# Performance work log

Measured on AMD Instinct MI355X. Metric: run time of the kernel, lower is better.

## Reference

```python
import jax, jax.numpy as jnp
import numpy as np

ALPHA = 2.0   # snntorch ATan surrogate default
THRESH = 1.0  # snntorch Leaky default threshold

@jax.custom_vjp
def spike(x):
    return (x > 0).astype(x.dtype)

def _spike_fwd(x):
    return spike(x), x

def _spike_bwd(x, g):
    # ATan surrogate gradient: (alpha/2) / (1 + (pi/2 * alpha * x)^2)
    return (g * (ALPHA / 2) / (1 + (jnp.pi / 2 * ALPHA * x) ** 2),)

spike.defvjp(_spike_fwd, _spike_bwd)

def _lif(inp, mem, beta):
    # snntorch Leaky, reset_mechanism='subtract':
    # reset from previous mem (detached), then integrate, then fire
    reset = jax.lax.stop_gradient(spike(mem - THRESH))
    mem = jnp.clip(beta, 0.0, 1.0) * mem + inp - reset * THRESH
    spk = spike(mem - THRESH)
    return spk, mem

def setup_inputs() -> dict:
    key = jax.random.key(0)
    ks = jax.random.split(key, 8)
    V, H, T, B = 32000, 512, 512, 8
    s = 0.02
    inv = 1.0 / np.sqrt(H)
    return {
        "x": jax.random.randint(ks[0], (T, B), 0, V),
        "emb": jax.random.normal(ks[1], (V, H), jnp.float32) * s,
        "pos_emb": jax.random.normal(ks[2], (T, H), jnp.float32) * s,
        "beta1": jnp.full((H,), 0.9, jnp.float32),
        "beta2": jnp.full((H,), 0.9, jnp.float32),
        "beta3": jnp.full((H,), 0.9, jnp.float32),
        "W2": jax.random.normal(ks[3], (H, H), jnp.float32) * inv,
        "b2": jnp.zeros((H,), jnp.float32),
        "W3": jax.random.normal(ks[4], (H, H), jnp.float32) * inv,
        "b3": jnp.zeros((H,), jnp.float32),
        "Wout": jax.random.normal(ks[5], (V, H), jnp.float32) * inv,
        "bout": jnp.zeros((V,), jnp.float32),
    }

def reference(x, emb, pos_emb, beta1, beta2, beta3, W2, b2, W3, b3, Wout, bout):
    T, B = x.shape
    H = emb.shape[1]
    # precompute token + positional embedding for all steps: [T, B, H]
    hid = emb[x] + pos_emb[:, None, :]
    mem0 = jnp.zeros((B, H), emb.dtype)

    def step(carry, h_t):
        m1, m2, m3 = carry
        spk1, m1 = _lif(h_t, m1, beta1)
        h = jax.nn.relu(spk1 @ W2.T + b2)
        spk2, m2 = _lif(h, m2, beta2)
        h = jax.nn.relu(spk2 @ W3.T + b3)
        spk3, m3 = _lif(h, m3, beta3)
        logits = spk3 @ Wout.T + bout  # [B, V]
        return (m1, m2, m3), logits

    _, out = jax.lax.scan(step, (mem0, mem0, mem0), hid)
    return out  # [T, B, V]
```

## Files before the change

### kernel.cpp

```cpp
#include <hip/hip_runtime.h>

#define TT 512
#define BB 8
#define HH 512
#define VV 32000
#define RR (TT * BB)

typedef float v4f __attribute__((ext_vector_type(4)));

__device__ __forceinline__ float clip01(float x) { return fminf(fmaxf(x, 0.0f), 1.0f); }

__global__ void __launch_bounds__(512) snn_scan_kernel(
        const int* __restrict__ x, const float* __restrict__ emb,
        const float* __restrict__ pos,
        const float* __restrict__ beta1, const float* __restrict__ beta2,
        const float* __restrict__ beta3,
        const float* __restrict__ W2, const float* __restrict__ b2,
        const float* __restrict__ W3, const float* __restrict__ b3,
        int* __restrict__ act1, int* __restrict__ act2, int* __restrict__ act3,
        int* __restrict__ cnt3_g) {
    __shared__ int x_lds[TT];
    __shared__ int c1[TT], c2[TT], c3[TT];
    const int b = blockIdx.x;
    const int h = threadIdx.x;

    x_lds[h] = x[h * BB + b];
    c1[h] = 0; c2[h] = 0; c3[h] = 0;
    __syncthreads();

    {
        float bt = clip01(beta1[h]);
        float m = 0.0f;
        for (int t0 = 0; t0 < TT; t0 += 32) {
            float ev[32], pv[32];
#pragma unroll
            for (int u = 0; u < 32; ++u) {
                int xv = x_lds[t0 + u];
                ev[u] = emb[((size_t)xv << 9) + h];
                pv[u] = pos[((t0 + u) << 9) + h];
            }
#pragma unroll
            for (int u = 0; u < 32; ++u) {
                float inp = ev[u] + pv[u];
                float reset = (m > 1.0f) ? 1.0f : 0.0f;
                m = bt * m + inp - reset;
                if (m > 1.0f) {
                    int t = t0 + u;
                    int p = atomicAdd(&c1[t], 1);
                    act1[((t * BB + b) << 9) + p] = h;
                }
            }
        }
    }
    __syncthreads();

    {
        float bh = b2[h];
        float inp0 = fmaxf(bh, 0.0f);
        float bt = clip01(beta2[h]);
        float m = 0.0f;
        for (int t0 = 0; t0 < TT; t0 += 16) {
            int n[16];
#pragma unroll
            for (int u = 0; u < 16; ++u) n[u] = c1[t0 + u];
#pragma unroll
            for (int u = 0; u < 16; ++u) {
                float inp;
                if (n[u] == 0) {
                    inp = inp0;
                } else {
                    float acc = bh;
                    const int* a = act1 + (((t0 + u) * BB + b) << 9);
                    for (int i = 0; i < n[u]; ++i) acc += W2[(h << 9) + a[i]];
                    inp = fmaxf(acc, 0.0f);
                }
                float reset = (m > 1.0f) ? 1.0f : 0.0f;
                m = bt * m + inp - reset;
                if (m > 1.0f) {
                    int t = t0 + u;
                    int p = atomicAdd(&c2[t], 1);
                    act2[((t * BB + b) << 9) + p] = h;
                }
            }
        }
    }
    __syncthreads();

    {
        float bh = b3[h];
        float inp0 = fmaxf(bh, 0.0f);
        float bt = clip01(beta3[h]);
        float m = 0.0f;
        for (int t0 = 0; t0 < TT; t0 += 16) {
            int n[16];
#pragma unroll
            for (int u = 0; u < 16; ++u) n[u] = c2[t0 + u];
#pragma unroll
            for (int u = 0; u < 16; ++u) {
                float inp;
                if (n[u] == 0) {
                    inp = inp0;
                } else {
                    float acc = bh;
                    const int* a = act2 + (((t0 + u) * BB + b) << 9);
                    for (int i = 0; i < n[u]; ++i) acc += W3[(h << 9) + a[i]];
                    inp = fmaxf(acc, 0.0f);
                }
                float reset = (m > 1.0f) ? 1.0f : 0.0f;
                m = bt * m + inp - reset;
                if (m > 1.0f) {
                    int t = t0 + u;
                    int p = atomicAdd(&c3[t], 1);
                    act3[((t * BB + b) << 9) + p] = h;
                }
            }
        }
    }
    __syncthreads();
    cnt3_g[h * BB + b] = c3[h];
}

#define ROWS_PER_BLK 8

__global__ void __launch_bounds__(512) out_gemm_kernel(
        const int* __restrict__ cnt, const int* __restrict__ act,
        const float* __restrict__ Wout, const float* __restrict__ bout,
        float* __restrict__ out) {
    const int tid = threadIdx.x;
    const int v0 = tid * 4;

    float4 bv[16];
#pragma unroll
    for (int k = 0; k < 16; ++k) {
        int v = v0 + k * 2048;
        if (v < VV) bv[k] = *(const float4*)(bout + v);
    }

    const int r0 = blockIdx.x * ROWS_PER_BLK;
#pragma unroll
    for (int rr = 0; rr < ROWS_PER_BLK; ++rr) {
        const int r = r0 + rr;
        const int n = cnt[r];
        float* __restrict__ orow = out + (size_t)r * VV;
        if (n == 0) {
#pragma unroll
            for (int k = 0; k < 16; ++k) {
                int v = v0 + k * 2048;
                if (v < VV) {
                    v4f st = {bv[k].x, bv[k].y, bv[k].z, bv[k].w};
                    __builtin_nontemporal_store(st, (v4f*)(orow + v));
                }
            }
        } else {
            const int* __restrict__ a = act + (r << 9);
#pragma unroll
            for (int k = 0; k < 16; ++k) {
                int v = v0 + k * 2048;
                if (v < VV) {
                    float4 acc = bv[k];
                    for (int i = 0; i < n; ++i) {
                        int kk = a[i];
                        acc.x += Wout[(size_t)(v + 0) * HH + kk];
                        acc.y += Wout[(size_t)(v + 1) * HH + kk];
                        acc.z += Wout[(size_t)(v + 2) * HH + kk];
                        acc.w += Wout[(size_t)(v + 3) * HH + kk];
                    }
                    v4f st = {acc.x, acc.y, acc.z, acc.w};
                    __builtin_nontemporal_store(st, (v4f*)(orow + v));
                }
            }
        }
    }
}

extern "C" void kernel_launch(void* const* d_in, const int* in_sizes, int n_in,
                              void* d_out, int out_size, void* d_ws, size_t ws_size,
                              hipStream_t stream) {
    const int*   x     = (const int*)d_in[0];
    const float* emb   = (const float*)d_in[1];
    const float* pos   = (const float*)d_in[2];
    const float* beta1 = (const float*)d_in[3];
    const float* beta2 = (const float*)d_in[4];
    const float* beta3 = (const float*)d_in[5];
    const float* W2    = (const float*)d_in[6];
    const float* b2    = (const float*)d_in[7];
    const float* W3    = (const float*)d_in[8];
    const float* b3    = (const float*)d_in[9];
    const float* Wout  = (const float*)d_in[10];
    const float* bout  = (const float*)d_in[11];
    float* out = (float*)d_out;

    int* act1 = (int*)d_ws;
    int* act2 = act1 + (size_t)RR * HH;
    int* act3 = act2 + (size_t)RR * HH;
    int* cnt3 = act3 + (size_t)RR * HH;

    snn_scan_kernel<<<BB, HH, 0, stream>>>(x, emb, pos, beta1, beta2, beta3,
                                           W2, b2, W3, b3, act1, act2, act3, cnt3);
    out_gemm_kernel<<<RR / ROWS_PER_BLK, HH, 0, stream>>>(cnt3, act3, Wout, bout, out);
}
```

Measured before the change: 688.9 us.

## Split fused LIF scan into per-layer kernels across hidden-dimension chunks

Replaces the single 8-block scan kernel with three per-layer kernels. Each kernel launches 64 blocks of 64 threads, splitting the hidden dimension into 8 chunks per batch element so more compute units take part. Spike counts move from LDS atomics to global atomics, zeroed by a memset, and the layers are separated by kernel boundaries instead of block barriers. This adds launch overhead and global atomic contention, and spike list order now depends on inter-block timing.

```diff
diff --git a/kernel.cpp b/kernel.cpp
--- a/kernel.cpp
+++ b/kernel.cpp
@@ -5,119 +5,90 @@
 #define HH 512
 #define VV 32000
 #define RR (TT * BB)
+#define HC 8
+#define CHUNK (HH / HC)
 
 typedef float v4f __attribute__((ext_vector_type(4)));
 
 __device__ __forceinline__ float clip01(float x) { return fminf(fmaxf(x, 0.0f), 1.0f); }
 
-__global__ void __launch_bounds__(512) snn_scan_kernel(
+__global__ void __launch_bounds__(64) lif1_kernel(
         const int* __restrict__ x, const float* __restrict__ emb,
-        const float* __restrict__ pos,
-        const float* __restrict__ beta1, const float* __restrict__ beta2,
-        const float* __restrict__ beta3,
-        const float* __restrict__ W2, const float* __restrict__ b2,
-        const float* __restrict__ W3, const float* __restrict__ b3,
-        int* __restrict__ act1, int* __restrict__ act2, int* __restrict__ act3,
-        int* __restrict__ cnt3_g) {
+        const float* __restrict__ pos, const float* __restrict__ beta1,
+        int* __restrict__ act1, int* __restrict__ cnt1) {
     __shared__ int x_lds[TT];
-    __shared__ int c1[TT], c2[TT], c3[TT];
-    const int b = blockIdx.x;
-    const int h = threadIdx.x;
-
-    x_lds[h] = x[h * BB + b];
-    c1[h] = 0; c2[h] = 0; c3[h] = 0;
+    const int b  = blockIdx.x & 7;
+    const int hc = blockIdx.x >> 3;
+    const int tid = threadIdx.x;
+    for (int i = tid; i < TT; i += 64) x_lds[i] = x[i * BB + b];
     __syncthreads();
 
-    {
-        float bt = clip01(beta1[h]);
-        float m = 0.0f;
-        for (int t0 = 0; t0 < TT; t0 += 32) {
-            float ev[32], pv[32];
+    const int h = hc * CHUNK + tid;
+    const float bt = clip01(beta1[h]);
+    float m = 0.0f;
+    for (int t0 = 0; t0 < TT; t0 += 32) {
+        float ev[32], pv[32];
 #pragma unroll
-            for (int u = 0; u < 32; ++u) {
-                int xv = x_lds[t0 + u];
-                ev[u] = emb[((size_t)xv << 9) + h];
-                pv[u] = pos[((t0 + u) << 9) + h];
-            }
+        for (int u = 0; u < 32; ++u) {
+            int xv = x_lds[t0 + u];
+            ev[u] = emb[((size_t)xv << 9) + h];
+            pv[u] = pos[((t0 + u) << 9) + h];
+        }
 #pragma unroll
-            for (int u = 0; u < 32; ++u) {
-                float inp = ev[u] + pv[u];
-                float reset = (m > 1.0f) ? 1.0f : 0.0f;
-                m = bt * m + inp - reset;
-                if (m > 1.0f) {
-                    int t = t0 + u;
-                    int p = atomicAdd(&c1[t], 1);
-                    act1[((t * BB + b) << 9) + p] = h;
-                }
+        for (int u = 0; u < 32; ++u) {
+            float inp = ev[u] + pv[u];
+            float reset = (m > 1.0f) ? 1.0f : 0.0f;
+            m = bt * m + inp - reset;
+            if (m > 1.0f) {
+                int t = t0 + u;
+                int p = atomicAdd(&cnt1[t * BB + b], 1);
+                act1[((t * BB + b) << 9) + p] = h;
             }
         }
     }
+}
+
+__global__ void __launch_bounds__(64) lifh_kernel(
+        const float* __restrict__ W, const float* __restrict__ bvec,
+        const float* __restrict__ beta,
+        const int* __restrict__ cnt_in, const int* __restrict__ act_in,
+        int* __restrict__ act_out, int* __restrict__ cnt_out) {
+    __shared__ int c_lds[TT];
+    const int b  = blockIdx.x & 7;
+    const int hc = blockIdx.x >> 3;
+    const int tid = threadIdx.x;
+    for (int i = tid; i < TT; i += 64) c_lds[i] = cnt_in[i * BB + b];
     __syncthreads();
 
-    {
-        float bh = b2[h];
-        float inp0 = fmaxf(bh, 0.0f);
-        float bt = clip01(beta2[h]);
-        float m = 0.0f;
-        for (int t0 = 0; t0 < TT; t0 += 16) {
-            int n[16];
+    const int h = hc * CHUNK + tid;
+    const float bh = bvec[h];
+    const float inp0 = fmaxf(bh, 0.0f);
+    const float bt = clip01(beta[h]);
+    float m = 0.0f;
+    for (int t0 = 0; t0 < TT; t0 += 16) {
+        int n[16];
 #pragma unroll
-            for (int u = 0; u < 16; ++u) n[u] = c1[t0 + u];
+        for (int u = 0; u < 16; ++u) n[u] = c_lds[t0 + u];
 #pragma unroll
-            for (int u = 0; u < 16; ++u) {
-                float inp;
-                if (n[u] == 0) {
-                    inp = inp0;
-                } else {
-                    float acc = bh;
-                    const int* a = act1 + (((t0 + u) * BB + b) << 9);
-                    for (int i = 0; i < n[u]; ++i) acc += W2[(h << 9) + a[i]];
-                    inp = fmaxf(acc, 0.0f);
-                }
-                float reset = (m > 1.0f) ? 1.0f : 0.0f;
-                m = bt * m + inp - reset;
-                if (m > 1.0f) {
-                    int t = t0 + u;
-                    int p = atomicAdd(&c2[t], 1);
-                    act2[((t * BB + b) << 9) + p] = h;
-                }
+        for (int u = 0; u < 16; ++u) {
+            float inp;
+            if (n[u] == 0) {
+                inp = inp0;
+            } else {
+                float acc = bh;
+                const int* a = act_in + (((t0 + u) * BB + b) << 9);
+                for (int i = 0; i < n[u]; ++i) acc += W[(h << 9) + a[i]];
+                inp = fmaxf(acc, 0.0f);
+            }
+            float reset = (m > 1.0f) ? 1.0f : 0.0f;
+            m = bt * m + inp - reset;
+            if (m > 1.0f) {
+                int t = t0 + u;
+                int p = atomicAdd(&cnt_out[t * BB + b], 1);
+                act_out[((t * BB + b) << 9) + p] = h;
             }
         }
     }
-    __syncthreads();
-
-    {
-        float bh = b3[h];
-        float inp0 = fmaxf(bh, 0.0f);
-        float bt = clip01(beta3[h]);
-        float m = 0.0f;
-        for (int t0 = 0; t0 < TT; t0 += 16) {
-            int n[16];
-#pragma unroll
-            for (int u = 0; u < 16; ++u) n[u] = c2[t0 + u];
-#pragma unroll
-            for (int u = 0; u < 16; ++u) {
-                float inp;
-                if (n[u] == 0) {
-                    inp = inp0;
-                } else {
-                    float acc = bh;
-                    const int* a = act2 + (((t0 + u) * BB + b) << 9);
-                    for (int i = 0; i < n[u]; ++i) acc += W3[(h << 9) + a[i]];
-                    inp = fmaxf(acc, 0.0f);
-                }
-                float reset = (m > 1.0f) ? 1.0f : 0.0f;
-                m = bt * m + inp - reset;
-                if (m > 1.0f) {
-                    int t = t0 + u;
-                    int p = atomicAdd(&c3[t], 1);
-                    act3[((t * BB + b) << 9) + p] = h;
-                }
-            }
-        }
-    }
-    __syncthreads();
-    cnt3_g[h * BB + b] = c3[h];
 }
 
 #define ROWS_PER_BLK 8
@@ -193,9 +164,14 @@
     int* act1 = (int*)d_ws;
     int* act2 = act1 + (size_t)RR * HH;
     int* act3 = act2 + (size_t)RR * HH;
-    int* cnt3 = act3 + (size_t)RR * HH;
+    int* cnt1 = act3 + (size_t)RR * HH;
+    int* cnt2 = cnt1 + RR;
+    int* cnt3 = cnt2 + RR;
 
-    snn_scan_kernel<<<BB, HH, 0, stream>>>(x, emb, pos, beta1, beta2, beta3,
-                                           W2, b2, W3, b3, act1, act2, act3, cnt3);
+    hipMemsetAsync(cnt1, 0, 3 * RR * sizeof(int), stream);
+
+    lif1_kernel<<<BB * HC, CHUNK, 0, stream>>>(x, emb, pos, beta1, act1, cnt1);
+    lifh_kernel<<<BB * HC, CHUNK, 0, stream>>>(W2, b2, beta2, cnt1, act1, act2, cnt2);
+    lifh_kernel<<<BB * HC, CHUNK, 0, stream>>>(W3, b3, beta3, cnt2, act2, act3, cnt3);
     out_gemm_kernel<<<RR / ROWS_PER_BLK, HH, 0, stream>>>(cnt3, act3, Wout, bout, out);
 }
```

After: 688.4 us. No clear change (-0.1%).
